# Optimization experiments

Measured on AMD Instinct MI355X. Metric: run time of the kernel, lower is better.

## Reference

```python
import jax, jax.numpy as jnp
import numpy as np

N = 16384
D = 512
K = 1024          # fixed num_clusters (torch code uses randint(2, N//2))
NUM_ITERS = 10    # kmeans Lloyd iterations
NUM_CLUSTER_ITERS = 1
TEMPERATURE = 0.1
CONCENTRATION = 0.1
EPS = 1e-6


def setup_inputs() -> dict:
    key = jax.random.key(0)
    feats = jax.random.normal(key, (N, D), dtype=jnp.float32)
    return {"feats": feats}


def _assign(feats, centroids, x_sq):
    c_sq = jnp.sum(centroids * centroids, axis=-1)            # [K]
    d = x_sq[:, None] - 2.0 * (feats @ centroids.T) + c_sq[None, :]
    return jnp.argmin(d, axis=-1)                             # [N] int32


def _kmeans(feats, num_clusters, num_iters):
    x_sq = jnp.sum(feats * feats, axis=-1)                    # [N]
    init_centroids = feats[:num_clusters]                     # deterministic init

    def body(_, centroids):
        clusters = _assign(feats, centroids, x_sq)
        sums = jax.ops.segment_sum(feats, clusters, num_segments=num_clusters)
        counts = jax.ops.segment_sum(jnp.ones((feats.shape[0],), feats.dtype),
                                     clusters, num_segments=num_clusters)
        new_c = sums / jnp.maximum(counts, 1.0)[:, None]
        # keep old centroid for empty clusters
        return jnp.where(counts[:, None] > 0, new_c, centroids)

    centroids = jax.lax.fori_loop(0, num_iters, body, init_centroids)
    clusters = _assign(feats, centroids, x_sq)
    counts = jax.ops.segment_sum(jnp.ones((feats.shape[0],), feats.dtype),
                                 clusters, num_segments=num_clusters)
    return clusters, centroids, counts


def reference(feats):
    clusters, centroids, _ = _kmeans(feats, K, NUM_ITERS)
    # per-point squared residuals gathered by cluster id, scatter-added to [K, D]
    resid2 = (feats - centroids[clusters]) ** 2               # [N, D]
    dists = jax.ops.segment_sum(resid2, clusters, num_segments=K)  # [K, D]
    # entropy loss branch (concentration phi)
    p = jnp.exp(-dists / CONCENTRATION)
    Q = p / jnp.sum(p)
    entropy = jnp.mean(Q * jnp.log(Q + EPS)) / NUM_CLUSTER_ITERS
    # nll branch (temperature t)
    p2 = jnp.exp(-dists / TEMPERATURE)
    nll = -jnp.mean(jnp.log(p2 + EPS))
    return entropy + nll
```

## Files before the change

kernel.cpp:

```cpp
#include <hip/hip_runtime.h>
#include <math.h>

#define N 16384
#define D 512
#define K 1024
#define NUM_ITERS 10
#define TEMPERATURE 0.1f
#define CONCENTRATION 0.1f
#define EPS 1e-6f

typedef unsigned short ushort_t;
typedef unsigned int uint_t;
typedef unsigned long long u64;
typedef __attribute__((ext_vector_type(4))) float floatx4;
typedef __attribute__((ext_vector_type(8))) short shortx8;

__device__ inline ushort_t f2h(float f) {
    _Float16 h = (_Float16)f;
    return *(ushort_t*)&h;
}

__device__ inline unsigned ford(float f) {
    unsigned b = __float_as_uint(f);
    return (b & 0x80000000u) ? ~b : (b | 0x80000000u);
}

__device__ inline void f4add(float4& a, const float4& b) {
    a.x += b.x; a.y += b.y; a.z += b.z; a.w += b.w;
}

__device__ inline void gld16(const void* g, void* l) {
    __builtin_amdgcn_global_load_lds(
        (const __attribute__((address_space(1))) void*)(uintptr_t)(g),
        (__attribute__((address_space(3))) void*)(uintptr_t)(l), 16, 0, 0);
}

#define WAITVM(n_lit) asm volatile("s_waitcnt vmcnt(" #n_lit ")" ::: "memory")

#define SPLIT_BLOCKS (N * D / 4 / 256)
__global__ void split_kernel(const float* __restrict__ x, ushort_t* __restrict__ hi,
                             u64* __restrict__ best2, float* __restrict__ cent,
                             double* __restrict__ scal, float* __restrict__ csq) {
    const int bid = blockIdx.x;
    const int tid = threadIdx.x;
    if (bid < SPLIT_BLOCKS) {
        int i = bid * 256 + tid;
        float4 v = ((const float4*)x)[i];
        ushort4 hv = {f2h(v.x), f2h(v.y), f2h(v.z), f2h(v.w)};
        ((ushort4*)hi)[i] = hv;
        if (i < 2 * N) best2[i] = ~0ull;
        if (i < K * D / 4) ((float4*)cent)[i] = v;
        if (i == 0) { scal[0] = 0.0; scal[1] = 0.0; scal[2] = 0.0; *(int*)&scal[3] = 0; }
    } else {
        int row = (bid - SPLIT_BLOCKS) * 4 + (tid >> 6);
        int lane = tid & 63;
        if (row >= K) return;
        const float* r = x + (size_t)row * D;
        float s = 0.f;
        for (int i = lane; i < D; i += 64) { float v = r[i]; s += v * v; }
        for (int off = 32; off > 0; off >>= 1) s += __shfl_down(s, off, 64);
        if (lane == 0) csq[row] = s;
    }
}

__global__ __launch_bounds__(512, 2) void assign_mfma2(
    const ushort_t* __restrict__ Ah, const ushort_t* __restrict__ Bh,
    const float* __restrict__ csq, u64* __restrict__ best)
{
    __shared__ __align__(16) ushort_t sA[4][8192];
    __shared__ __align__(16) ushort_t sB[4][8192];

    const int tid = threadIdx.x;
    const int lane = tid & 63;
    const int wave = tid >> 6;
    const int wr = wave >> 2, wc = wave & 3;
    const int quad = lane >> 4, l16 = lane & 15;

    const int bid = (int)blockIdx.x;
    const int xid = bid & 7;
    const int s = bid >> 3;
    const int brow = (xid << 3) + (s >> 2);
    const int bcol = s & 3;
    const int row0 = brow * 256, col0 = bcol * 256;

    floatx4 acc[8][4];
#pragma unroll
    for (int a = 0; a < 8; ++a)
#pragma unroll
        for (int b = 0; b < 4; ++b) acc[a][b] = (floatx4){0.f, 0.f, 0.f, 0.f};

    const int swz = (quad ^ (l16 & 3) ^ ((l16 >> 2) & 3)) * 8;
    const int aoff = (wr * 128 + l16) * 32 + swz;
    const int boff = (wc * 64 + l16) * 32 + swz;

    auto stage = [&](int h) {
        const int u_h = h >> 2;
        const int part = h & 3;
        const int kh = part >> 1;
        const int reg = ((u_h & 1) << 1) | kh;
        const int d_off = u_h * 64 + kh * 32;
        const ushort_t* src = (part & 1) ? Bh : Ah;
        const int r0 = (part & 1) ? col0 : row0;
        ushort_t* dstreg = ((part & 1) ? &sB[0][0] : &sA[0][0]) + reg * 8192;
#pragma unroll
        for (int ii = 0; ii < 2; ++ii) {
            const int idx = ii * 512 + tid;
            const int row = idx >> 2;
            const int kb = (idx & 3) ^ (row & 3) ^ ((row >> 2) & 3);
            gld16(src + (size_t)(r0 + row) * D + d_off + kb * 8, dstreg + idx * 8);
        }
    };

    #pragma unroll
    for (int h = 0; h < 6; ++h) stage(h);
    WAITVM(8);
    __builtin_amdgcn_s_barrier();
    __builtin_amdgcn_sched_barrier(0);

    shortx8 fb[4];
#pragma unroll
    for (int u = 0; u < 8; ++u) {
        const int rbase = (u & 1) << 1;
#pragma unroll
        for (int p = 0; p < 4; ++p) {
            const int g = u * 4 + p;
            if (g + 6 < 32) stage(g + 6);
            const int kh = p >> 1;
            const int ih = p & 1;
            const ushort_t* Areg = &sA[0][0] + (rbase + kh) * 8192;
            const ushort_t* Breg = &sB[0][0] + (rbase + kh) * 8192;
            shortx8 fa[4];
            if (ih == 0) {
#pragma unroll
                for (int j = 0; j < 4; ++j) fb[j] = *(const shortx8*)&Breg[boff + j * 512];
            }
#pragma unroll
            for (int i = 0; i < 4; ++i) fa[i] = *(const shortx8*)&Areg[aoff + (ih * 4 + i) * 512];
            __builtin_amdgcn_s_setprio(1);
#pragma unroll
            for (int i = 0; i < 4; ++i)
#pragma unroll
                for (int j = 0; j < 4; ++j)
                    acc[ih * 4 + i][j] = __builtin_amdgcn_mfma_f32_16x16x32_f16(
                        fa[i], fb[j], acc[ih * 4 + i][j], 0, 0, 0);
            __builtin_amdgcn_s_setprio(0);
            if ((p == 1 || p == 3) && !(u == 7 && p == 3)) {
                asm volatile("s_waitcnt lgkmcnt(0)" ::: "memory");
                if (u == 7 && p == 1)      { WAITVM(0); }
                else if (u == 6 && p == 3) { WAITVM(4); }
                else                       { WAITVM(8); }
                __builtin_amdgcn_s_barrier();
                __builtin_amdgcn_sched_barrier(0);
            }
        }
    }

    float csqv[4];
#pragma unroll
    for (int j = 0; j < 4; ++j) csqv[j] = csq[col0 + wc * 64 + j * 16 + l16];

    const int k0 = col0 + wc * 64 + l16;
#pragma unroll
    for (int i = 0; i < 8; ++i) {
#pragma unroll
        for (int r = 0; r < 4; ++r) {
            float bv = csqv[0] - 2.0f * acc[i][0][r];
            int bk = k0;
#pragma unroll
            for (int j = 1; j < 4; ++j) {
                float v = csqv[j] - 2.0f * acc[i][j][r];
                int kk = k0 + j * 16;
                if (v < bv || (v == bv && kk < bk)) { bv = v; bk = kk; }
            }
#pragma unroll
            for (int m = 1; m < 16; m <<= 1) {
                float ov = __shfl_xor(bv, m, 64);
                int ok = __shfl_xor(bk, m, 64);
                if (ov < bv || (ov == bv && ok < bk)) { bv = ov; bk = ok; }
            }
            if (l16 == 0) {
                int p = row0 + wr * 128 + i * 16 + quad * 4 + r;
                u64 pk = ((u64)ford(bv) << 32) | (unsigned)bk;
                atomicMin(&best[p], pk);
            }
        }
    }
}

#define CU_WAVES 8
#define CHUNKS (N / 128)
#define ROUNDS 4
#define WIN (CHUNKS / ROUNDS)
#define CPW (WIN / CU_WAVES)

__global__ __launch_bounds__(512) void cluster_update(
    const float* __restrict__ feats, const u64* __restrict__ best,
    u64* __restrict__ best_other,
    float* __restrict__ cent, ushort_t* __restrict__ Bh,
    float* __restrict__ csq)
{
    __shared__ int list[CU_WAVES][CPW * 128];
    __shared__ int lcnt[CU_WAVES];
    __shared__ float4 part[CU_WAVES][64][2];
    __shared__ int pcnt_s[CU_WAVES];

    const int tid = threadIdx.x;
    const int lane = tid & 63;
    const int wave = tid >> 6;
    const int k = (int)blockIdx.x;

    float4 a0 = {0.f, 0.f, 0.f, 0.f}, a1 = {0.f, 0.f, 0.f, 0.f};
    int cnttot = 0;

    for (int round = 0; round < ROUNDS; ++round) {
        int cw = 0;
#pragma unroll
        for (int cc = 0; cc < CPW; ++cc) {
            int chunk = round * WIN + wave * CPW + cc;
            ulonglong2 v = ((const ulonglong2*)best)[chunk * 64 + lane];
            int id0 = (int)(uint_t)v.x;
            int id1 = (int)(uint_t)v.y;
            int p0 = chunk * 128 + 2 * lane;
            u64 m0 = __ballot(id0 == k);
            u64 m1 = __ballot(id1 == k);
            int c0 = __popcll(m0);
            u64 lanem = (1ull << lane) - 1ull;
            if (id0 == k) list[wave][cw + __popcll(m0 & lanem)] = p0;
            if (id1 == k) list[wave][cw + c0 + __popcll(m1 & lanem)] = p0 + 1;
            cw += c0 + __popcll(m1);
        }
        if (lane == 0) lcnt[wave] = cw;
        cnttot += cw;
        __syncthreads();

        int off[CU_WAVES]; int T = 0;
#pragma unroll
        for (int j = 0; j < CU_WAVES; ++j) { off[j] = T; T += lcnt[j]; }

        for (int g0 = wave; g0 < T; g0 += CU_WAVES * 4) {
            int nb = 0; int pidx[4];
#pragma unroll
            for (int b = 0; b < 4; ++b) {
                int g = g0 + CU_WAVES * b;
                if (g < T) {
                    int j = 0;
#pragma unroll
                    for (int jj = 1; jj < CU_WAVES; ++jj) if (g >= off[jj]) j = jj;
                    pidx[nb++] = list[j][g - off[j]];
                }
            }
            float4 x[4][2];
#pragma unroll
            for (int b = 0; b < 4; ++b) if (b < nb) {
                const float4* r = (const float4*)(feats + (size_t)pidx[b] * D) + lane * 2;
                x[b][0] = r[0]; x[b][1] = r[1];
            }
#pragma unroll
            for (int b = 0; b < 4; ++b) if (b < nb) {
                f4add(a0, x[b][0]); f4add(a1, x[b][1]);
            }
        }
        __syncthreads();
    }

    part[wave][lane][0] = a0; part[wave][lane][1] = a1;
    if (lane == 0) pcnt_s[wave] = cnttot;
    __syncthreads();

    if (wave == 0) {
        float4 s0 = part[0][lane][0], s1 = part[0][lane][1];
        int c = pcnt_s[0];
#pragma unroll
        for (int w = 1; w < CU_WAVES; ++w) {
            f4add(s0, part[w][lane][0]); f4add(s1, part[w][lane][1]);
            c += pcnt_s[w];
        }

        float4* crow = (float4*)(cent + (size_t)k * D) + lane * 2;
        float4 c0, c1;
        if (c > 0) {
            float cf = (float)c;
            c0 = (float4){s0.x / cf, s0.y / cf, s0.z / cf, s0.w / cf};
            c1 = (float4){s1.x / cf, s1.y / cf, s1.z / cf, s1.w / cf};
        } else {
            c0 = crow[0]; c1 = crow[1];
        }
        crow[0] = c0; crow[1] = c1;

        ushort4 hv;
        hv.x = f2h(c0.x); hv.y = f2h(c0.y); hv.z = f2h(c0.z); hv.w = f2h(c0.w);
        ((ushort4*)(Bh + (size_t)k * D))[lane * 2] = hv;
        hv.x = f2h(c1.x); hv.y = f2h(c1.y); hv.z = f2h(c1.z); hv.w = f2h(c1.w);
        ((ushort4*)(Bh + (size_t)k * D))[lane * 2 + 1] = hv;

        float s = c0.x * c0.x + c0.y * c0.y + c0.z * c0.z + c0.w * c0.w
                + c1.x * c1.x + c1.y * c1.y + c1.z * c1.z + c1.w * c1.w;
        for (int o = 32; o > 0; o >>= 1) s += __shfl_xor(s, o, 64);
        if (lane == 0) csq[k] = s;
    }

    if (tid < 16) best_other[k * 16 + tid] = ~0ull;
}

__global__ __launch_bounds__(512) void dist_gather(
    const float* __restrict__ feats, const float* __restrict__ cent,
    const u64* __restrict__ best, float* __restrict__ dists)
{
    __shared__ int list[CU_WAVES][CPW * 128];
    __shared__ int lcnt[CU_WAVES];
    __shared__ float4 part[CU_WAVES][64][2];

    const int tid = threadIdx.x;
    const int lane = tid & 63;
    const int wave = tid >> 6;
    const int k = (int)blockIdx.x;

    const float4* crow = (const float4*)(cent + (size_t)k * D) + lane * 2;
    const float4 c0 = crow[0], c1 = crow[1];

    float4 a0 = {0.f, 0.f, 0.f, 0.f}, a1 = {0.f, 0.f, 0.f, 0.f};

    for (int round = 0; round < ROUNDS; ++round) {
        int cw = 0;
#pragma unroll
        for (int cc = 0; cc < CPW; ++cc) {
            int chunk = round * WIN + wave * CPW + cc;
            ulonglong2 v = ((const ulonglong2*)best)[chunk * 64 + lane];
            int id0 = (int)(uint_t)v.x;
            int id1 = (int)(uint_t)v.y;
            int p0 = chunk * 128 + 2 * lane;
            u64 m0 = __ballot(id0 == k);
            u64 m1 = __ballot(id1 == k);
            int cc0 = __popcll(m0);
            u64 lanem = (1ull << lane) - 1ull;
            if (id0 == k) list[wave][cw + __popcll(m0 & lanem)] = p0;
            if (id1 == k) list[wave][cw + cc0 + __popcll(m1 & lanem)] = p0 + 1;
            cw += cc0 + __popcll(m1);
        }
        if (lane == 0) lcnt[wave] = cw;
        __syncthreads();

        int off[CU_WAVES]; int T = 0;
#pragma unroll
        for (int j = 0; j < CU_WAVES; ++j) { off[j] = T; T += lcnt[j]; }

        for (int g0 = wave; g0 < T; g0 += CU_WAVES * 4) {
            int nb = 0; int pidx[4];
#pragma unroll
            for (int b = 0; b < 4; ++b) {
                int g = g0 + CU_WAVES * b;
                if (g < T) {
                    int j = 0;
#pragma unroll
                    for (int jj = 1; jj < CU_WAVES; ++jj) if (g >= off[jj]) j = jj;
                    pidx[nb++] = list[j][g - off[j]];
                }
            }
            float4 x[4][2];
#pragma unroll
            for (int b = 0; b < 4; ++b) if (b < nb) {
                const float4* r = (const float4*)(feats + (size_t)pidx[b] * D) + lane * 2;
                x[b][0] = r[0]; x[b][1] = r[1];
            }
#pragma unroll
            for (int b = 0; b < 4; ++b) if (b < nb) {
                float r;
                r = x[b][0].x - c0.x; a0.x += r * r;  r = x[b][0].y - c0.y; a0.y += r * r;
                r = x[b][0].z - c0.z; a0.z += r * r;  r = x[b][0].w - c0.w; a0.w += r * r;
                r = x[b][1].x - c1.x; a1.x += r * r;  r = x[b][1].y - c1.y; a1.y += r * r;
                r = x[b][1].z - c1.z; a1.z += r * r;  r = x[b][1].w - c1.w; a1.w += r * r;
            }
        }
        __syncthreads();
    }

    part[wave][lane][0] = a0; part[wave][lane][1] = a1;
    __syncthreads();
    if (wave == 0) {
        float4 s0 = part[0][lane][0], s1 = part[0][lane][1];
#pragma unroll
        for (int w = 1; w < CU_WAVES; ++w) { f4add(s0, part[w][lane][0]); f4add(s1, part[w][lane][1]); }
        float4* drow = (float4*)(dists + (size_t)k * D) + lane * 2;
        drow[0] = s0; drow[1] = s1;
    }
}

__global__ void loss_fused(const float* __restrict__ dists, double* __restrict__ scal,
                           float* __restrict__ out) {
    const int tid = threadIdx.x;
    int* cnt = (int*)&scal[3];
    __shared__ float red[4];
    __shared__ double Sbc;

    float v = 0.f;
    for (int idx = blockIdx.x * 256 + tid; idx < K * D; idx += 256 * 256)
        v += expf(-(dists[idx] / CONCENTRATION));
    for (int off = 32; off > 0; off >>= 1) v += __shfl_down(v, off, 64);
    if ((tid & 63) == 0) red[tid >> 6] = v;
    __syncthreads();
    if (tid == 0) {
        atomicAdd(&scal[0], (double)(red[0] + red[1] + red[2] + red[3]));
        __threadfence();
        atomicAdd(cnt, 1);
        while (atomicAdd(cnt, 0) < 256) __builtin_amdgcn_s_sleep(1);
        Sbc = atomicAdd(&scal[0], 0.0);
    }
    __syncthreads();
    const float S = (float)Sbc;

    float e = 0.f, nl = 0.f;
    for (int idx = blockIdx.x * 256 + tid; idx < K * D; idx += 256 * 256) {
        float dv = dists[idx];
        float p = expf(-(dv / CONCENTRATION));
        float qq = p / S;
        e += qq * logf(qq + EPS);
        float p2 = expf(-(dv / TEMPERATURE));
        nl += logf(p2 + EPS);
    }
    __shared__ float rede[4];
    __shared__ float redn[4];
    for (int off = 32; off > 0; off >>= 1) { e += __shfl_down(e, off, 64); nl += __shfl_down(nl, off, 64); }
    if ((tid & 63) == 0) { rede[tid >> 6] = e; redn[tid >> 6] = nl; }
    __syncthreads();
    if (tid == 0) {
        atomicAdd(&scal[1], (double)(rede[0] + rede[1] + rede[2] + rede[3]));
        atomicAdd(&scal[2], (double)(redn[0] + redn[1] + redn[2] + redn[3]));
        __threadfence();
        int t = atomicAdd(cnt, 1);
        if (t == 511) {
            double e_s = atomicAdd(&scal[1], 0.0);
            double n_s = atomicAdd(&scal[2], 0.0);
            double kd = (double)(K * D);
            double entropy = e_s / kd;
            double nll = -(n_s / kd);
            out[0] = (float)(entropy + nll);
        }
    }
}

extern "C" void kernel_launch(void* const* d_in, const int* in_sizes, int n_in,
                              void* d_out, int out_size, void* d_ws, size_t ws_size,
                              hipStream_t stream) {
    const float* feats = (const float*)d_in[0];
    float* out = (float*)d_out;

    ushort_t* Ah = (ushort_t*)d_ws;
    ushort_t* Bh = Ah + (size_t)N * D;
    float* centroids = (float*)(Bh + (size_t)K * D);
    float* dists     = centroids + (size_t)K * D;
    float* csq       = dists + (size_t)K * D;
    u64*   best0     = (u64*)(csq + K);
    u64*   best1     = best0 + N;
    double* scal     = (double*)(best1 + N);

    split_kernel<<<SPLIT_BLOCKS + K / 4, 256, 0, stream>>>(feats, Ah, best0, centroids,
                                                           scal, csq);

    for (int it = 0; it < NUM_ITERS; ++it) {
        u64* cur = (it & 1) ? best1 : best0;
        u64* oth = (it & 1) ? best0 : best1;
        const ushort_t* bh = (it == 0) ? Ah : Bh;
        assign_mfma2<<<(N / 256) * (K / 256), 512, 0, stream>>>(Ah, bh, csq, cur);
        cluster_update<<<K, 512, 0, stream>>>(feats, cur, oth, centroids, Bh, csq);
    }
    u64* fin = (NUM_ITERS & 1) ? best1 : best0;
    assign_mfma2<<<(N / 256) * (K / 256), 512, 0, stream>>>(Ah, Bh, csq, fin);

    dist_gather<<<K, 512, 0, stream>>>(feats, centroids, fin, dists);

    loss_fused<<<256, 256, 0, stream>>>(dists, scal, out);
}
```

Baseline: 703.5 us.

## Shrink assign GEMM tile to 256x128 with 3-stage pipeline and higher occupancy

Replaces the 256x256 assign kernel with a 256x128 tile per block. Each wave now owns a 64x64 sub-tile, and K-slices of 32 are staged through a triple-buffered LDS ring instead of the previous 4-region half-step scheme. Grid size doubles and launch bounds ask for 4 blocks per CU, aiming at better occupancy and latency hiding while cutting accumulator registers and LDS per block. The trade-off is lower arithmetic intensity per block: B is reused across fewer rows, A is re-read twice as often, and there are more barriers per unit of MFMA work.

```diff
diff --git a/kernel.cpp b/kernel.cpp
--- a/kernel.cpp
+++ b/kernel.cpp
@@ -63,95 +63,84 @@
     }
 }
 
-__global__ __launch_bounds__(512, 2) void assign_mfma2(
+__global__ __launch_bounds__(512, 4) void assign_mfma3(
     const ushort_t* __restrict__ Ah, const ushort_t* __restrict__ Bh,
     const float* __restrict__ csq, u64* __restrict__ best)
 {
-    __shared__ __align__(16) ushort_t sA[4][8192];
-    __shared__ __align__(16) ushort_t sB[4][8192];
+    __shared__ __align__(16) ushort_t sA[3 * 8192];
+    __shared__ __align__(16) ushort_t sB[3 * 4096];
 
     const int tid = threadIdx.x;
     const int lane = tid & 63;
     const int wave = tid >> 6;
-    const int wr = wave >> 2, wc = wave & 3;
+    const int wr = wave >> 1, wc = wave & 1;
     const int quad = lane >> 4, l16 = lane & 15;
 
     const int bid = (int)blockIdx.x;
     const int xid = bid & 7;
     const int s = bid >> 3;
-    const int brow = (xid << 3) + (s >> 2);
-    const int bcol = s & 3;
-    const int row0 = brow * 256, col0 = bcol * 256;
-
-    floatx4 acc[8][4];
-#pragma unroll
-    for (int a = 0; a < 8; ++a)
+    const int brow = (xid << 3) + (s >> 3);
+    const int bcol = s & 7;
+    const int row0 = brow * 256, col0 = bcol * 128;
+
+    floatx4 acc[4][4];
+#pragma unroll
+    for (int a = 0; a < 4; ++a)
 #pragma unroll
         for (int b = 0; b < 4; ++b) acc[a][b] = (floatx4){0.f, 0.f, 0.f, 0.f};
 
     const int swz = (quad ^ (l16 & 3) ^ ((l16 >> 2) & 3)) * 8;
-    const int aoff = (wr * 128 + l16) * 32 + swz;
+    const int aoff = (wr * 64 + l16) * 32 + swz;
     const int boff = (wc * 64 + l16) * 32 + swz;
 
-    auto stage = [&](int h) {
-        const int u_h = h >> 2;
-        const int part = h & 3;
-        const int kh = part >> 1;
-        const int reg = ((u_h & 1) << 1) | kh;
-        const int d_off = u_h * 64 + kh * 32;
-        const ushort_t* src = (part & 1) ? Bh : Ah;
-        const int r0 = (part & 1) ? col0 : row0;
-        ushort_t* dstreg = ((part & 1) ? &sB[0][0] : &sA[0][0]) + reg * 8192;
+    auto stage = [&](int t2) {
+        const int r = t2 % 3;
+        ushort_t* dA = sA + r * 8192;
+        ushort_t* dB = sB + r * 4096;
+        const int d0 = t2 * 32;
 #pragma unroll
         for (int ii = 0; ii < 2; ++ii) {
             const int idx = ii * 512 + tid;
             const int row = idx >> 2;
             const int kb = (idx & 3) ^ (row & 3) ^ ((row >> 2) & 3);
-            gld16(src + (size_t)(r0 + row) * D + d_off + kb * 8, dstreg + idx * 8);
+            gld16(Ah + (size_t)(row0 + row) * D + d0 + kb * 8, dA + idx * 8);
+        }
+        {
+            const int idx = tid;
+            const int row = idx >> 2;
+            const int kb = (idx & 3) ^ (row & 3) ^ ((row >> 2) & 3);
+            gld16(Bh + (size_t)(col0 + row) * D + d0 + kb * 8, dB + idx * 8);
         }
     };
 
-    #pragma unroll
-    for (int h = 0; h < 6; ++h) stage(h);
-    WAITVM(8);
+    stage(0); stage(1);
+    WAITVM(3);
     __builtin_amdgcn_s_barrier();
     __builtin_amdgcn_sched_barrier(0);
 
-    shortx8 fb[4];
-#pragma unroll
-    for (int u = 0; u < 8; ++u) {
-        const int rbase = (u & 1) << 1;
-#pragma unroll
-        for (int p = 0; p < 4; ++p) {
-            const int g = u * 4 + p;
-            if (g + 6 < 32) stage(g + 6);
-            const int kh = p >> 1;
-            const int ih = p & 1;
-            const ushort_t* Areg = &sA[0][0] + (rbase + kh) * 8192;
-            const ushort_t* Breg = &sB[0][0] + (rbase + kh) * 8192;
-            shortx8 fa[4];
-            if (ih == 0) {
-#pragma unroll
-                for (int j = 0; j < 4; ++j) fb[j] = *(const shortx8*)&Breg[boff + j * 512];
-            }
-#pragma unroll
-            for (int i = 0; i < 4; ++i) fa[i] = *(const shortx8*)&Areg[aoff + (ih * 4 + i) * 512];
-            __builtin_amdgcn_s_setprio(1);
-#pragma unroll
-            for (int i = 0; i < 4; ++i)
-#pragma unroll
-                for (int j = 0; j < 4; ++j)
-                    acc[ih * 4 + i][j] = __builtin_amdgcn_mfma_f32_16x16x32_f16(
-                        fa[i], fb[j], acc[ih * 4 + i][j], 0, 0, 0);
-            __builtin_amdgcn_s_setprio(0);
-            if ((p == 1 || p == 3) && !(u == 7 && p == 3)) {
-                asm volatile("s_waitcnt lgkmcnt(0)" ::: "memory");
-                if (u == 7 && p == 1)      { WAITVM(0); }
-                else if (u == 6 && p == 3) { WAITVM(4); }
-                else                       { WAITVM(8); }
-                __builtin_amdgcn_s_barrier();
-                __builtin_amdgcn_sched_barrier(0);
-            }
+#pragma unroll
+    for (int t = 0; t < 16; ++t) {
+        if (t + 2 < 16) stage(t + 2);
+        const ushort_t* Ar = sA + (t % 3) * 8192;
+        const ushort_t* Br = sB + (t % 3) * 4096;
+        shortx8 fa[4], fb[4];
+#pragma unroll
+        for (int j = 0; j < 4; ++j) fb[j] = *(const shortx8*)&Br[boff + j * 512];
+#pragma unroll
+        for (int i = 0; i < 4; ++i) fa[i] = *(const shortx8*)&Ar[aoff + i * 512];
+        __builtin_amdgcn_s_setprio(1);
+#pragma unroll
+        for (int i = 0; i < 4; ++i)
+#pragma unroll
+            for (int j = 0; j < 4; ++j)
+                acc[i][j] = __builtin_amdgcn_mfma_f32_16x16x32_f16(
+                    fa[i], fb[j], acc[i][j], 0, 0, 0);
+        __builtin_amdgcn_s_setprio(0);
+        if (t < 15) {
+            asm volatile("s_waitcnt lgkmcnt(0)" ::: "memory");
+            if (t < 14) { WAITVM(3); } else { WAITVM(0); }
+            __builtin_amdgcn_s_barrier();
+            __builtin_amdgcn_sched_barrier(0);
         }
     }
 
@@ -161,7 +150,7 @@
 
     const int k0 = col0 + wc * 64 + l16;
 #pragma unroll
-    for (int i = 0; i < 8; ++i) {
+    for (int i = 0; i < 4; ++i) {
 #pragma unroll
         for (int r = 0; r < 4; ++r) {
             float bv = csqv[0] - 2.0f * acc[i][0][r];
@@ -179,7 +168,7 @@
                 if (ov < bv || (ov == bv && ok < bk)) { bv = ov; bk = ok; }
             }
             if (l16 == 0) {
-                int p = row0 + wr * 128 + i * 16 + quad * 4 + r;
+                int p = row0 + wr * 64 + i * 16 + quad * 4 + r;
                 u64 pk = ((u64)ford(bv) << 32) | (unsigned)bk;
                 atomicMin(&best[p], pk);
             }
@@ -460,11 +449,11 @@
         u64* cur = (it & 1) ? best1 : best0;
         u64* oth = (it & 1) ? best0 : best1;
         const ushort_t* bh = (it == 0) ? Ah : Bh;
-        assign_mfma2<<<(N / 256) * (K / 256), 512, 0, stream>>>(Ah, bh, csq, cur);
+        assign_mfma3<<<(N / 256) * (K / 128), 512, 0, stream>>>(Ah, bh, csq, cur);
         cluster_update<<<K, 512, 0, stream>>>(feats, cur, oth, centroids, Bh, csq);
     }
     u64* fin = (NUM_ITERS & 1) ? best1 : best0;
-    assign_mfma2<<<(N / 256) * (K / 256), 512, 0, stream>>>(Ah, Bh, csq, fin);
+    assign_mfma3<<<(N / 256) * (K / 128), 512, 0, stream>>>(Ah, Bh, csq, fin);
 
     dist_gather<<<K, 512, 0, stream>>>(feats, centroids, fin, dists);
 
```

Result: faster. 672.8 us (median of 3 runs) (-4.4%).
